# Kernel tuning notes

Hardware: AMD Instinct MI355X
Metric: run time of the kernel (lower is better)

## Reference

```python
import jax, jax.numpy as jnp
import numpy as np

B, L, D = 4, 4096, 1024
DFF = 4 * D
CAPACITY = 0.5
K = int(L * CAPACITY)  # 2048 tokens kept per sequence


def setup_inputs() -> dict:
    key = jax.random.key(0)
    ks = jax.random.split(key, 6)
    s = 0.02
    return {
        "x": jax.random.normal(ks[0], (B, L, D), dtype=jnp.float32),
        "W1": jax.random.normal(ks[1], (D, DFF), dtype=jnp.float32) * s,
        "b1": jnp.zeros((DFF,), dtype=jnp.float32),
        "W2": jax.random.normal(ks[2], (DFF, D), dtype=jnp.float32) * s,
        "b2": jnp.zeros((D,), dtype=jnp.float32),
        "wr": jax.random.normal(ks[3], (D,), dtype=jnp.float32) * s,
        "br": jnp.zeros((), dtype=jnp.float32),
    }


def reference(x, W1, b1, W2, b2, wr, br):
    # Router logits: Linear(D, 1) -> [B, L]
    scores = jnp.einsum("bld,d->bl", x, wr) + br
    # Hard top-k token selection (capacity_ratio * L tokens), sorted as in torch
    _, idx = jax.lax.top_k(scores, K)          # [B, K]
    idx = jnp.sort(idx, axis=1)
    # Gather selected tokens
    x_sel = jnp.take_along_axis(x, idx[:, :, None], axis=1)  # [B, K, D]
    # Inner MLP on the gathered subset (standard FFN: D -> 4D GELU -> D)
    h = jax.nn.gelu(jnp.einsum("bkd,df->bkf", x_sel, W1) + b1)
    y_sel = jnp.einsum("bkf,fd->bkd", h, W2) + b2            # [B, K, D]
    # Scatter back into a zero tensor of the full shape
    out = jnp.zeros_like(x)
    out = out.at[jnp.arange(B)[:, None], idx].set(y_sel)
    return out
```

## Files before the change

kernel.cpp:

```cpp
#include <hip/hip_runtime.h>
#include <hip/hip_bf16.h>

#define B_   4
#define L_   4096
#define D_   1024
#define DFF_ 4096
#define K_   2048

typedef __attribute__((ext_vector_type(8))) short bf16x8;
typedef __attribute__((ext_vector_type(4))) float f32x4;
typedef unsigned short u16;

__device__ __forceinline__ u16 f2bf(float f) {
    unsigned u = __float_as_uint(f);
    u += 0x7fffu + ((u >> 16) & 1u);
    return (u16)(u >> 16);
}

__device__ __forceinline__ float gelu_fast(float v) {
    float z = 1.5957691216057308f * v * (1.0f + 0.044715f * v * v);
    float e = __builtin_amdgcn_exp2f(-1.4426950408889634f * z);
    return v * __builtin_amdgcn_rcpf(1.0f + e);
}

__device__ __forceinline__ void gload_lds16(const void* g, void* l) {
    __builtin_amdgcn_global_load_lds(
        (const __attribute__((address_space(1))) void*)g,
        (__attribute__((address_space(3))) void*)l, 16, 0, 0);
}

template<int N> __device__ __forceinline__ void wait_vm() {
    if constexpr (N == 0) asm volatile("s_waitcnt vmcnt(0)" ::: "memory");
    else if constexpr (N == 3) asm volatile("s_waitcnt vmcnt(3)" ::: "memory");
    else if constexpr (N == 4) asm volatile("s_waitcnt vmcnt(4)" ::: "memory");
    __builtin_amdgcn_sched_barrier(0);
}

__global__ __launch_bounds__(256) void prep_kernel(
    const float* __restrict__ x, const float* __restrict__ wr,
    const float* __restrict__ br, float* __restrict__ scores,
    const float* __restrict__ W1, const float* __restrict__ W2,
    u16* __restrict__ W1T, u16* __restrict__ W2T)
{
    __shared__ float t[32][33];
    const int bb = blockIdx.x;
    if (bb < 4096) {
        int gtid  = bb * 256 + threadIdx.x;
        int token = gtid >> 6;
        int lane  = threadIdx.x & 63;
        const float* xr = x + (size_t)token * D_;
        double acc = 0.0;
        #pragma unroll
        for (int i = 0; i < 4; ++i) {
            int off = (lane + i * 64) * 4;
            float4 xv = *(const float4*)(xr + off);
            float4 wv = *(const float4*)(wr + off);
            acc += (double)xv.x * wv.x + (double)xv.y * wv.y +
                   (double)xv.z * wv.z + (double)xv.w * wv.w;
        }
        #pragma unroll
        for (int off = 32; off > 0; off >>= 1)
            acc += __shfl_down(acc, off);
        if (lane == 0) scores[token] = (float)(acc + (double)br[0]);
        return;
    }
    const float* in; u16* outb; int RK, RN, bx, by;
    if (bb < 8192) {
        int i = bb - 4096; in = W1; outb = W1T; RK = D_; RN = DFF_;
        bx = i & 127; by = i >> 7;
    } else {
        int i = bb - 8192; in = W2; outb = W2T; RK = DFF_; RN = D_;
        bx = i & 31; by = i >> 5;
    }
    int n0 = bx * 32, k0 = by * 32;
    int tx = threadIdx.x & 31, ty = threadIdx.x >> 5;
    #pragma unroll
    for (int i = 0; i < 4; ++i)
        t[ty + 8 * i][tx] = in[(size_t)(k0 + ty + 8 * i) * RN + (n0 + tx)];
    __syncthreads();
    #pragma unroll
    for (int i = 0; i < 4; ++i)
        outb[(size_t)(n0 + ty + 8 * i) * RK + (k0 + tx)] = f2bf(t[tx][ty + 8 * i]);
}

__global__ __launch_bounds__(256) void rank_zero_kernel(
    const float* __restrict__ scores, int* __restrict__ sel,
    float* __restrict__ out)
{
    __shared__ float sc[L_];
    __shared__ int selLds[64];
    const int b = blockIdx.y;
    const int t = threadIdx.x;
    const float* sb = scores + b * L_;
    for (int i = t; i < L_; i += 256) sc[i] = sb[i];
    __syncthreads();
    const int tg  = t >> 2;
    const int sub = t & 3;
    const int l   = blockIdx.x * 64 + tg;
    const float s = sc[l];
    int cnt = 0;
    const float4* sc4 = (const float4*)sc;
    const int base4 = sub * 256;
    for (int j4 = 0; j4 < 256; ++j4) {
        float4 v = sc4[base4 + j4];
        int j = (base4 + j4) * 4;
        cnt += (int)((v.x > s) || (v.x == s && (j + 0) < l));
        cnt += (int)((v.y > s) || (v.y == s && (j + 1) < l));
        cnt += (int)((v.z > s) || (v.z == s && (j + 2) < l));
        cnt += (int)((v.w > s) || (v.w == s && (j + 3) < l));
    }
    cnt += __shfl_xor(cnt, 1);
    cnt += __shfl_xor(cnt, 2);
    const int issel = (cnt < K_) ? 1 : 0;
    if (sub == 0) { sel[b * L_ + l] = issel; selLds[tg] = issel; }
    __syncthreads();
    float* obase = out + ((size_t)b * L_ + (size_t)blockIdx.x * 64) * D_;
    const float4 z = make_float4(0.f, 0.f, 0.f, 0.f);
    for (int r = 0; r < 64; ++r)
        if (!selLds[r])
            *(float4*)(obase + (size_t)r * D_ + t * 4) = z;
}

__global__ __launch_bounds__(256) void compact_kernel(
    const int* __restrict__ sel, int* __restrict__ idx)
{
    __shared__ int psum[256];
    int b = blockIdx.x, t = threadIdx.x;
    const int* sb = sel + b * L_;
    int base = t * 16;
    int flags[16]; int c = 0;
    #pragma unroll
    for (int i = 0; i < 16; ++i) { flags[i] = sb[base + i]; c += flags[i]; }
    psum[t] = c;
    __syncthreads();
    if (t == 0) {
        int acc = 0;
        for (int j = 0; j < 256; ++j) { int v = psum[j]; psum[j] = acc; acc += v; }
    }
    __syncthreads();
    int p = psum[t];
    #pragma unroll
    for (int i = 0; i < 16; ++i)
        if (flags[i]) idx[b * K_ + (p++)] = base + i;
}

__global__ __launch_bounds__(256) void gather_bf16_kernel(
    const float* __restrict__ x, const int* __restrict__ idxg,
    int row0, u16* __restrict__ xsel)
{
    int rl = blockIdx.x;
    int grow = row0 + rl;
    int tok = idxg[grow];
    int bb = grow >> 11;
    const float* src = x + ((size_t)bb * L_ + (size_t)tok) * D_;
    int t = threadIdx.x;
    float4 v = *(const float4*)(src + t * 4);
    ushort4 o;
    o.x = f2bf(v.x); o.y = f2bf(v.y); o.z = f2bf(v.z); o.w = f2bf(v.w);
    *(ushort4*)(xsel + (size_t)rl * D_ + t * 4) = o;
}

template<int BM, int KD, int EPI>
__global__ __launch_bounds__(512, 2) void gemm_8ph_kernel(
    const u16* __restrict__ A, const u16* __restrict__ Bm,
    const float* __restrict__ bias, u16* __restrict__ hout,
    float* __restrict__ outp, const int* __restrict__ idxg, int row0)
{
    constexpr int BN    = 256;
    constexpr int NT    = KD / 64;
    constexpr int M_REP = BM / 32;
    constexpr int PH    = (BM == 256) ? 8 : 4;
    constexpr int SPP   = 8 / PH;
    constexpr int IFL   = BM / 128 + 2;

    __shared__ u16 SH[(BM + BN) * 128];
    u16* SA = SH;
    u16* SB = SH + BM * 128;

    const int tid  = threadIdx.x;
    const int lane = tid & 63;
    const int wid  = tid >> 6;
    const int wm = wid >> 2, wn = wid & 3;
    const int fr = lane & 15;
    const int cq = lane >> 4;
    const int rq = cq * 4;
    const int kqx = (cq ^ ((fr >> 1) & 3)) * 8;

    constexpr int gx = (EPI == 0 ? DFF_ : D_) / 256;
    const int nwg = gridDim.x;
    const int o   = blockIdx.x;
    const int swz = (o & 7) * (nwg >> 3) + (o >> 3);
    const int bn  = (swz % gx) * 256;
    const int bm  = (swz / gx) * BM;

    const int srow = tid >> 2;
    const int sc   = tid & 3;
    const int scg  = sc ^ ((srow >> 1) & 3);
    const u16* AbaseS = A  + (size_t)(bm + srow) * KD + scg * 8;
    const u16* BbaseS = Bm + (size_t)(bn + srow) * KD + scg * 8;

    f32x4 acc[M_REP][4];
    #pragma unroll
    for (int m = 0; m < M_REP; ++m)
        #pragma unroll
        for (int n = 0; n < 4; ++n) acc[m][n] = (f32x4)0.0f;

    auto stage = [&](int s) {
        int kt = s >> 2, j = s & 3;
        int d = kt & 1, h = j >> 1;
        int koff = kt * 64 + h * 32;
        if (j & 1) {
            u16* dst = SB + (d * 2 + h) * 8192 + tid * 8;
            gload_lds16(BbaseS + koff, dst);
            gload_lds16(BbaseS + koff + (size_t)128 * KD, dst + 4096);
        } else {
            u16* dst = SA + (d * 2 + h) * (BM * 32) + tid * 8;
            gload_lds16(AbaseS + koff, dst);
            if constexpr (BM == 256)
                gload_lds16(AbaseS + koff + (size_t)128 * KD, dst + 4096);
        }
    };

    #pragma unroll
    for (int s = 0; s < 6; ++s) stage(s);
    wait_vm<IFL>();
    __builtin_amdgcn_s_barrier();

    bf16x8 bfv[4];
    for (int i = 0; i < NT / 2; ++i) {
        #pragma unroll
        for (int p = 0; p < PH; ++p) {
            const int d   = (BM == 256) ? ((p >> 2) & 1) : ((p >> 1) & 1);
            const int kh  = (BM == 256) ? ((p >> 1) & 1) : (p & 1);
            const int mlo = (BM == 256) ? (p & 1) * 4 : 0;
            const bool readB = (BM == 128) || ((p & 1) == 0);
            const int slot = d * 2 + kh;
            if (readB) {
                #pragma unroll
                for (int n = 0; n < 4; ++n)
                    bfv[n] = *(const bf16x8*)(SB + slot * 8192 +
                              (wn * 64 + n * 16 + fr) * 32 + kqx);
            }
            bf16x8 af[4];
            #pragma unroll
            for (int q = 0; q < 4; ++q)
                af[q] = *(const bf16x8*)(SA + slot * (BM * 32) +
                          (wm * (BM / 2) + (mlo + q) * 16 + fr) * 32 + kqx);
            #pragma unroll
            for (int u = 0; u < SPP; ++u) {
                int s = 8 * i + SPP * p + 6 + u;
                if (s < 4 * NT) stage(s);
            }
            __builtin_amdgcn_s_barrier();
            asm volatile("s_waitcnt lgkmcnt(0)" ::: "memory");
            __builtin_amdgcn_sched_barrier(0);
            __builtin_amdgcn_s_setprio(1);
            #pragma unroll
            for (int q = 0; q < 4; ++q)
                #pragma unroll
                for (int n = 0; n < 4; ++n)
                    acc[mlo + q][n] = __builtin_amdgcn_mfma_f32_16x16x32_bf16(
                        af[q], bfv[n], acc[mlo + q][n], 0, 0, 0);
            __builtin_amdgcn_s_setprio(0);
            if (p == PH / 2 - 1) {
                if (i == NT / 2 - 1) wait_vm<0>(); else wait_vm<IFL>();
            } else if (p == PH - 1) {
                if (i < NT / 2 - 1) wait_vm<IFL>();
            }
            __builtin_amdgcn_s_barrier();
        }
    }

    if constexpr (EPI == 0) {
        u16* ct = SH;
        #pragma unroll
        for (int n = 0; n < 4; ++n) {
            const int col = wn * 64 + n * 16 + fr;
            const float bc = bias[bn + col];
            #pragma unroll
            for (int m = 0; m < M_REP; ++m) {
                const int rb = wm * (BM / 2) + m * 16 + rq;
                #pragma unroll
                for (int r = 0; r < 4; ++r) {
                    int row = rb + r;
                    int pc  = col ^ (((row >> 2) & 3) << 4);
                    ct[row * 256 + pc] = f2bf(gelu_fast(acc[m][n][r] + bc));
                }
            }
        }
        __syncthreads();
        const int chunk = tid & 31;
        const int rw    = tid >> 5;
        #pragma unroll
        for (int pass = 0; pass < 16; ++pass) {
            int row = pass * 16 + rw;
            int pb  = (chunk * 8) ^ (((row >> 2) & 3) << 4);
            bf16x8 v = *(const bf16x8*)(ct + row * 256 + pb);
            *(bf16x8*)(hout + (size_t)(bm + row) * DFF_ + bn + chunk * 8) = v;
        }
    } else {
        #pragma unroll
        for (int n = 0; n < 4; ++n) {
            const int col = bn + wn * 64 + n * 16 + fr;
            const float bc = bias[col];
            #pragma unroll
            for (int m = 0; m < M_REP; ++m) {
                const int rbase = bm + wm * (BM / 2) + m * 16 + rq;
                #pragma unroll
                for (int r = 0; r < 4; ++r) {
                    int grow = row0 + rbase + r;
                    int bb = grow >> 11;
                    int tok = idxg[grow];
                    outp[((size_t)bb * L_ + (size_t)tok) * D_ + col] =
                        acc[m][n][r] + bc;
                }
            }
        }
    }
}

extern "C" void kernel_launch(void* const* d_in, const int* in_sizes, int n_in,
                              void* d_out, int out_size, void* d_ws, size_t ws_size,
                              hipStream_t stream)
{
    const float* x  = (const float*)d_in[0];
    const float* W1 = (const float*)d_in[1];
    const float* b1 = (const float*)d_in[2];
    const float* W2 = (const float*)d_in[3];
    const float* b2 = (const float*)d_in[4];
    const float* wr = (const float*)d_in[5];
    const float* br = (const float*)d_in[6];
    float* out = (float*)d_out;

    char* ws = (char*)d_ws;
    int*   idx    = (int*)ws;
    float* scores = (float*)(ws + (32 << 10));
    int*   sel    = (int*)(ws + (96 << 10));
    u16* W1T = (u16*)(ws + (256 << 10));
    u16* W2T = W1T + (size_t)DFF_ * D_;

    size_t fixedB = (size_t)(256 << 10) + (size_t)DFF_ * D_ * 2 * 2;
    size_t avail  = ws_size > fixedB ? ws_size - fixedB : 0;
    int RC = (int)(avail / (size_t)(D_ * 2 + DFF_ * 2));
    RC = (RC / 256) * 256;
    if (RC > B_ * K_) RC = B_ * K_;
    if (RC < 256) RC = 256;
    u16* xsel = (u16*)(ws + fixedB);
    u16* hbuf = xsel + (size_t)RC * D_;

    prep_kernel<<<dim3(12288), 256, 0, stream>>>(x, wr, br, scores, W1, W2, W1T, W2T);
    rank_zero_kernel<<<dim3(L_ / 64, B_), 256, 0, stream>>>(scores, sel, out);
    compact_kernel<<<dim3(B_), 256, 0, stream>>>(sel, idx);

    for (int r0 = 0; r0 < B_ * K_; r0 += RC) {
        int rc = (B_ * K_ - r0 < RC) ? (B_ * K_ - r0) : RC;
        gather_bf16_kernel<<<dim3(rc), 256, 0, stream>>>(x, idx, r0, xsel);
        gemm_8ph_kernel<256, D_, 0><<<dim3((DFF_ / 256) * (rc / 256)), 512, 0, stream>>>(
            xsel, W1T, b1, hbuf, nullptr, nullptr, 0);
        gemm_8ph_kernel<128, DFF_, 1><<<dim3((D_ / 256) * (rc / 128)), 512, 0, stream>>>(
            hbuf, W2T, b2, nullptr, out, idx, r0);
    }
}
```

Baseline: 215.6 us.

## Double-buffer LDS fragment reads to overlap next phase loads with MFMA

Restructures the GEMM main loop so each phase prefetches the next phase's A/B fragments from LDS into a second register buffer before running the current phase's MFMAs. Partial lgkmcnt waits and retuned vmcnt waits replace the full lgkmcnt(0) wait and one of the two barriers per phase. The goal is to hide LDS read latency behind matrix math and cut barrier stalls. It costs extra VGPRs for the doubled fragment buffers, and the hand-tuned wait counts carry a correctness and race risk.

```diff
diff --git a/kernel.cpp b/kernel.cpp
--- a/kernel.cpp
+++ b/kernel.cpp
@@ -33,6 +33,14 @@
     if constexpr (N == 0) asm volatile("s_waitcnt vmcnt(0)" ::: "memory");
     else if constexpr (N == 3) asm volatile("s_waitcnt vmcnt(3)" ::: "memory");
     else if constexpr (N == 4) asm volatile("s_waitcnt vmcnt(4)" ::: "memory");
+    else if constexpr (N == 6) asm volatile("s_waitcnt vmcnt(6)" ::: "memory");
+    else if constexpr (N == 8) asm volatile("s_waitcnt vmcnt(8)" ::: "memory");
+    __builtin_amdgcn_sched_barrier(0);
+}
+
+template<int N> __device__ __forceinline__ void wait_lgkm() {
+    if constexpr (N == 4) asm volatile("s_waitcnt lgkmcnt(4)" ::: "memory");
+    else                  asm volatile("s_waitcnt lgkmcnt(8)" ::: "memory");
     __builtin_amdgcn_sched_barrier(0);
 }
 
@@ -168,10 +176,10 @@
 {
     constexpr int BN    = 256;
     constexpr int NT    = KD / 64;
+    constexpr int NI    = NT / 2;
     constexpr int M_REP = BM / 32;
     constexpr int PH    = (BM == 256) ? 8 : 4;
     constexpr int SPP   = 8 / PH;
-    constexpr int IFL   = BM / 128 + 2;
 
     __shared__ u16 SH[(BM + BN) * 128];
     u16* SA = SH;
@@ -204,6 +212,9 @@
     for (int m = 0; m < M_REP; ++m)
         #pragma unroll
         for (int n = 0; n < 4; ++n) acc[m][n] = (f32x4)0.0f;
+
+    bf16x8 af[2][4];
+    bf16x8 bfv[2][4];
 
     auto stage = [&](int s) {
         int kt = s >> 2, j = s & 3;
@@ -223,53 +234,69 @@
 
     #pragma unroll
     for (int s = 0; s < 6; ++s) stage(s);
-    wait_vm<IFL>();
+    if constexpr (BM == 256) wait_vm<8>(); else wait_vm<6>();
     __builtin_amdgcn_s_barrier();
 
-    bf16x8 bfv[4];
-    for (int i = 0; i < NT / 2; ++i) {
-        #pragma unroll
-        for (int p = 0; p < PH; ++p) {
-            const int d   = (BM == 256) ? ((p >> 2) & 1) : ((p >> 1) & 1);
-            const int kh  = (BM == 256) ? ((p >> 1) & 1) : (p & 1);
-            const int mlo = (BM == 256) ? (p & 1) * 4 : 0;
-            const bool readB = (BM == 128) || ((p & 1) == 0);
-            const int slot = d * 2 + kh;
-            if (readB) {
-                #pragma unroll
-                for (int n = 0; n < 4; ++n)
-                    bfv[n] = *(const bf16x8*)(SB + slot * 8192 +
-                              (wn * 64 + n * 16 + fr) * 32 + kqx);
-            }
-            bf16x8 af[4];
-            #pragma unroll
-            for (int q = 0; q < 4; ++q)
-                af[q] = *(const bf16x8*)(SA + slot * (BM * 32) +
-                          (wm * (BM / 2) + (mlo + q) * 16 + fr) * 32 + kqx);
-            #pragma unroll
-            for (int u = 0; u < SPP; ++u) {
-                int s = 8 * i + SPP * p + 6 + u;
-                if (s < 4 * NT) stage(s);
-            }
-            __builtin_amdgcn_s_barrier();
-            asm volatile("s_waitcnt lgkmcnt(0)" ::: "memory");
-            __builtin_amdgcn_sched_barrier(0);
-            __builtin_amdgcn_s_setprio(1);
-            #pragma unroll
-            for (int q = 0; q < 4; ++q)
-                #pragma unroll
-                for (int n = 0; n < 4; ++n)
-                    acc[mlo + q][n] = __builtin_amdgcn_mfma_f32_16x16x32_bf16(
-                        af[q], bfv[n], acc[mlo + q][n], 0, 0, 0);
-            __builtin_amdgcn_s_setprio(0);
-            if (p == PH / 2 - 1) {
-                if (i == NT / 2 - 1) wait_vm<0>(); else wait_vm<IFL>();
-            } else if (p == PH - 1) {
-                if (i < NT / 2 - 1) wait_vm<IFL>();
-            }
-            __builtin_amdgcn_s_barrier();
-        }
-    }
+#define RDF(q) { \
+    const int d_    = (PH == 8) ? (((q) >> 2) & 1) : (((q) >> 1) & 1); \
+    const int kh_   = (PH == 8) ? (((q) >> 1) & 1) : ((q) & 1); \
+    const int mlo_  = (PH == 8) ? ((q) & 1) * 4 : 0; \
+    const int slot_ = d_ * 2 + kh_; \
+    if (PH == 4 || ((q) & 1) == 0) { \
+        const int bb_ = (PH == 8) ? (((q) >> 1) & 1) : ((q) & 1); \
+        _Pragma("unroll") \
+        for (int n = 0; n < 4; ++n) \
+            bfv[bb_][n] = *(const bf16x8*)(SB + slot_ * 8192 + \
+                          (wn * 64 + n * 16 + fr) * 32 + kqx); \
+    } \
+    _Pragma("unroll") \
+    for (int q2 = 0; q2 < 4; ++q2) \
+        af[(q) & 1][q2] = *(const bf16x8*)(SA + slot_ * (BM * 32) + \
+                          (wm * (BM / 2) + (mlo_ + q2) * 16 + fr) * 32 + kqx); \
+}
+
+    RDF(0)
+
+#define PHASE(p) { \
+    _Pragma("unroll") \
+    for (int u = 0; u < SPP; ++u) { \
+        int s = 8 * i + SPP * (p) + 6 + u; \
+        if (s < 4 * NT) stage(s); \
+    } \
+    RDF(((p) + 1) % PH) \
+    if (PH == 4 || ((((p) + 1) % PH) & 1) == 0) wait_lgkm<8>(); else wait_lgkm<4>(); \
+    __builtin_amdgcn_s_setprio(1); \
+    { const int mlo_ = (PH == 8) ? ((p) & 1) * 4 : 0; \
+      const int bi_  = (PH == 8) ? (((p) >> 1) & 1) : ((p) & 1); \
+      _Pragma("unroll") \
+      for (int q2 = 0; q2 < 4; ++q2) \
+          _Pragma("unroll") \
+          for (int n = 0; n < 4; ++n) \
+              acc[mlo_ + q2][n] = __builtin_amdgcn_mfma_f32_16x16x32_bf16( \
+                  af[(p) & 1][q2], bfv[bi_][n], acc[mlo_ + q2][n], 0, 0, 0); } \
+    __builtin_amdgcn_s_setprio(0); \
+    if constexpr (PH == 8) { \
+        if ((p) == 2)      { if (lastI) wait_vm<4>(); else wait_vm<6>(); } \
+        else if ((p) == 4) { if (lastI) wait_vm<0>(); else wait_vm<6>(); } \
+        else                 wait_vm<6>(); \
+    } else { \
+        if ((p) == 0)        wait_vm<3>(); \
+        else               { if (lastI) wait_vm<0>(); else wait_vm<3>(); } \
+    } \
+    __builtin_amdgcn_s_barrier(); \
+}
+
+    for (int i = 0; i < NI; ++i) {
+        const bool lastI = (i == NI - 1);
+        if constexpr (PH == 8) {
+            PHASE(0) PHASE(1) PHASE(2) PHASE(3)
+            PHASE(4) PHASE(5) PHASE(6) PHASE(7)
+        } else {
+            PHASE(0) PHASE(1) PHASE(2) PHASE(3)
+        }
+    }
+#undef PHASE
+#undef RDF
 
     if constexpr (EPI == 0) {
         u16* ct = SH;
```

After: 214.1 us. About the same (-0.7%).
